# Optimization experiments

Measured on AMD Instinct MI355X. Metric: run time of the kernel, lower is better.

Reference implementation:

```python
import jax, jax.numpy as jnp
import numpy as np

BN_EPS = 1e-5

def setup_inputs() -> dict:
    key = jax.random.key(0)
    ks = jax.random.split(key, 6)
    B, C, H, W, K = 16, 512, 64, 64, 32
    return {
        "x": jax.random.normal(ks[0], (B, C, H, W), dtype=jnp.float32),
        "conv_w": jax.random.normal(ks[1], (C, C), dtype=jnp.float32) * (1.0 / np.sqrt(C)),
        "conv_b": jax.random.normal(ks[2], (C,), dtype=jnp.float32) * 0.01,
        "codewords": jax.random.normal(ks[3], (K, C), dtype=jnp.float32) * (1.0 / np.sqrt(C)),
        "scale": jax.random.uniform(ks[4], (K,), dtype=jnp.float32, minval=-1.0, maxval=0.0),
        "bn_gamma": jnp.ones((K,), jnp.float32),
        "bn_beta": jnp.zeros((K,), jnp.float32),
        "bn_mean": jnp.zeros((K,), jnp.float32),
        "bn_var": jnp.ones((K,), jnp.float32),
        "fc_w": jax.random.normal(ks[5], (C, C), dtype=jnp.float32) * (1.0 / np.sqrt(C)),
        "fc_b": jnp.zeros((C,), jnp.float32),
    }

def reference(x, conv_w, conv_b, codewords, scale, bn_gamma, bn_beta, bn_mean, bn_var, fc_w, fc_b):
    B, C, H, W = x.shape
    N = H * W
    # 1x1 conv projection: (B,C,H,W) x (O,C) -> (B,O,H,W)
    proj = jnp.einsum('bchw,oc->bohw', x, conv_w) + conv_b[None, :, None, None]
    z = proj.reshape(B, C, N).transpose(0, 2, 1)  # (B, N, C)
    # scaled L2 distances without materializing (B,N,K,C):
    # ||z - cw||^2 = ||z||^2 - 2 z.cw + ||cw||^2
    z_sq = jnp.sum(z * z, axis=-1)                     # (B, N)
    cw_sq = jnp.sum(codewords * codewords, axis=-1)    # (K,)
    cross = jnp.einsum('bnc,kc->bnk', z, codewords)    # (B, N, K)
    dist = scale[None, None, :] * (z_sq[:, :, None] - 2.0 * cross + cw_sq[None, None, :])
    assign = jax.nn.softmax(dist, axis=2)              # (B, N, K)
    # aggregate: sum_n a[b,n,k] * (z[b,n,c] - cw[k,c])
    enc = jnp.einsum('bnk,bnc->bkc', assign, z) - jnp.sum(assign, axis=1)[:, :, None] * codewords[None]  # (B, K, C)
    # BatchNorm1d(num_codes) in eval mode normalizes the K (feature) axis, then ReLU
    inv_std = jax.lax.rsqrt(bn_var + BN_EPS)
    enc_bn = (enc - bn_mean[None, :, None]) * (inv_std * bn_gamma)[None, :, None] + bn_beta[None, :, None]
    encoding_feat = jnp.mean(jax.nn.relu(enc_bn), axis=1)  # (B, C)
    # sigmoid channel gate + residual fuse
    gamma = jax.nn.sigmoid(encoding_feat @ fc_w.T + fc_b)  # (B, C)
    y = gamma[:, :, None, None]
    output = jax.nn.relu(x + x * y)
    return (encoding_feat, output)
```

## Files before the change

### kernel.cpp

```cpp
#include <hip/hip_runtime.h>
#include <hip/hip_bf16.h>
#include <stdint.h>

#define DEV static __device__ __forceinline__

typedef __attribute__((ext_vector_type(8))) short bf16x8;
typedef __attribute__((ext_vector_type(4))) float f32x4;

DEV void async_ld16(const void* g, void* l) {
  __builtin_amdgcn_global_load_lds(
      (const __attribute__((address_space(1))) void*)g,
      (__attribute__((address_space(3))) void*)l, 16, 0, 0);
}

DEV unsigned short f2bf(float f) {
  union { __hip_bfloat16 h; unsigned short u; } c;
  c.h = __float2bfloat16(f);
  return c.u;
}

#define Bb 16
#define Cc 512
#define Nn 4096
#define Kk 32
#define NSPLIT 32

__global__ void k_castw(const float* __restrict__ a, __hip_bfloat16* __restrict__ o) {
  int i = blockIdx.x * 256 + threadIdx.x;
  o[i] = __float2bfloat16(a[i]);
}

__global__ void k_cw(const float* __restrict__ cw, __hip_bfloat16* __restrict__ cwb,
                     float* __restrict__ cwsq) {
  int k = blockIdx.x, lane = threadIdx.x;
  float s = 0.f;
#pragma unroll
  for (int j = 0; j < 8; ++j) {
    float v = cw[k * Cc + lane * 8 + j];
    cwb[k * Cc + lane * 8 + j] = __float2bfloat16(v);
    s += v * v;
  }
  for (int off = 32; off; off >>= 1) s += __shfl_down(s, off);
  if (lane == 0) cwsq[k] = s;
}

__global__ __launch_bounds__(256) void k_gemm_z(const float* __restrict__ X,
                                                const __hip_bfloat16* __restrict__ Bw,
                                                const float* __restrict__ bias,
                                                __hip_bfloat16* __restrict__ Z) {
  constexpr int LDA = 36;
  __shared__ __align__(16) unsigned short As[128 * LDA];
  __shared__ __align__(16) __hip_bfloat16 Bs[128 * 32];
  const int b = blockIdx.y;
  const int n0 = (blockIdx.x & 31) * 128;
  const int c0 = (blockIdx.x >> 5) * 128;
  const int tid = threadIdx.x;
  const int lane = tid & 63, wid = tid >> 6;
  const int wr = (wid >> 1) * 64, wc = (wid & 1) * 64;
  const int cg = tid & 7;
  const int ng = tid >> 3;
  const float* Xb = X + (size_t)b * Cc * Nn + n0 + ng * 4;
  const __hip_bfloat16* Bbp = Bw + (size_t)c0 * Cc;
  f32x4 acc[4][4] = {};
  for (int kt = 0; kt < 16; ++kt) {
    int k0 = kt * 32;
    __syncthreads();
#pragma unroll
    for (int j = 0; j < 2; ++j) {
      int li = tid + j * 256;
      int row = li >> 2, kc = (li & 3) * 8;
      async_ld16(Bbp + (size_t)row * Cc + k0 + kc, (char*)Bs + li * 16);
    }
    float vv[4][4];
#pragma unroll
    for (int i = 0; i < 4; ++i) {
      float4 t = *(const float4*)&Xb[(size_t)(k0 + cg * 4 + i) * Nn];
      vv[i][0] = t.x; vv[i][1] = t.y; vv[i][2] = t.z; vv[i][3] = t.w;
    }
#pragma unroll
    for (int j = 0; j < 4; ++j) {
      ushort4 w;
      w.x = f2bf(vv[0][j]);
      w.y = f2bf(vv[1][j]);
      w.z = f2bf(vv[2][j]);
      w.w = f2bf(vv[3][j]);
      *(ushort4*)&As[(ng * 4 + j) * LDA + cg * 4] = w;
    }
    __syncthreads();
    bf16x8 af[4], bfv[4];
#pragma unroll
    for (int m = 0; m < 4; ++m) {
      int base = (wr + m * 16 + (lane & 15)) * LDA + (lane >> 4) * 8;
      union { ushort4 u2[2]; bf16x8 v8; } t;
      t.u2[0] = *(const ushort4*)&As[base];
      t.u2[1] = *(const ushort4*)&As[base + 4];
      af[m] = t.v8;
    }
#pragma unroll
    for (int nf = 0; nf < 4; ++nf)
      bfv[nf] = *(const bf16x8*)&Bs[(wc + nf * 16 + (lane & 15)) * 32 + (lane >> 4) * 8];
#pragma unroll
    for (int m = 0; m < 4; ++m)
#pragma unroll
      for (int nf = 0; nf < 4; ++nf)
        acc[m][nf] = __builtin_amdgcn_mfma_f32_16x16x32_bf16(af[m], bfv[nf], acc[m][nf], 0, 0, 0);
  }
  __hip_bfloat16* Zb = Z + ((size_t)b * Nn + n0) * Cc + c0;
#pragma unroll
  for (int nf = 0; nf < 4; ++nf) {
    int col = wc + nf * 16 + (lane & 15);
    float bv = bias[c0 + col];
#pragma unroll
    for (int m = 0; m < 4; ++m) {
#pragma unroll
      for (int r = 0; r < 4; ++r) {
        int row = wr + m * 16 + (lane >> 4) * 4 + r;
        Zb[(size_t)row * Cc + col] = __float2bfloat16(acc[m][nf][r] + bv);
      }
    }
  }
}

__global__ __launch_bounds__(256) void k_cross(const __hip_bfloat16* __restrict__ Z,
                                               const __hip_bfloat16* __restrict__ CW,
                                               const float* __restrict__ scale,
                                               const float* __restrict__ cwsq,
                                               float* __restrict__ assign,
                                               float* __restrict__ asum) {
  __shared__ __align__(16) __hip_bfloat16 As[128 * 32];
  __shared__ __align__(16) __hip_bfloat16 Bs[32 * 32];
  __shared__ float s_zsq[128];
  __shared__ float s_asum[Kk];
  int b = blockIdx.y;
  int n0 = blockIdx.x * 128;
  int tid = threadIdx.x, lane = tid & 63, wid = tid >> 6;
  if (tid < Kk) s_asum[tid] = 0.f;
  const __hip_bfloat16* Ab = Z + ((size_t)b * Nn + n0) * Cc;
  f32x4 acc[2][2] = {};
  float sq = 0.f;
  for (int kt = 0; kt < 16; ++kt) {
    int k0 = kt * 32;
    __syncthreads();
#pragma unroll
    for (int j = 0; j < 2; ++j) {
      int li = tid + j * 256;
      int row = li >> 2, kc = (li & 3) * 8;
      async_ld16(Ab + (size_t)row * Cc + k0 + kc, (char*)As + li * 16);
    }
    if (tid < 128) {
      int row = tid >> 2, kc = (tid & 3) * 8;
      async_ld16(CW + (size_t)row * Cc + k0 + kc, (char*)Bs + tid * 16);
    }
    __syncthreads();
    {
      int row = tid >> 1, h = (tid & 1) * 16;
      const __hip_bfloat16* p = &As[row * 32 + h];
#pragma unroll
      for (int i = 0; i < 16; ++i) {
        float v = __bfloat162float(p[i]);
        sq += v * v;
      }
    }
    bf16x8 af[2], bfv[2];
#pragma unroll
    for (int m = 0; m < 2; ++m)
      af[m] = *(const bf16x8*)&As[(wid * 32 + m * 16 + (lane & 15)) * 32 + (lane >> 4) * 8];
#pragma unroll
    for (int nf = 0; nf < 2; ++nf)
      bfv[nf] = *(const bf16x8*)&Bs[(nf * 16 + (lane & 15)) * 32 + (lane >> 4) * 8];
#pragma unroll
    for (int m = 0; m < 2; ++m)
#pragma unroll
      for (int nf = 0; nf < 2; ++nf)
        acc[m][nf] = __builtin_amdgcn_mfma_f32_16x16x32_bf16(af[m], bfv[nf], acc[m][nf], 0, 0, 0);
  }
  sq += __shfl_xor(sq, 1);
  if ((tid & 1) == 0) s_zsq[tid >> 1] = sq;
  __syncthreads();
  float sc[2], cq[2];
#pragma unroll
  for (int nf = 0; nf < 2; ++nf) {
    sc[nf] = scale[nf * 16 + (lane & 15)];
    cq[nf] = cwsq[nf * 16 + (lane & 15)];
  }
  float asump0 = 0.f, asump1 = 0.f;
#pragma unroll
  for (int m = 0; m < 2; ++m) {
#pragma unroll
    for (int r = 0; r < 4; ++r) {
      int row = wid * 32 + m * 16 + (lane >> 4) * 4 + r;
      float zq = s_zsq[row];
      float v0 = sc[0] * (zq - 2.f * acc[m][0][r] + cq[0]);
      float v1 = sc[1] * (zq - 2.f * acc[m][1][r] + cq[1]);
      float mx = fmaxf(v0, v1);
#pragma unroll
      for (int off = 1; off < 16; off <<= 1) mx = fmaxf(mx, __shfl_xor(mx, off));
      float e0 = __expf(v0 - mx), e1 = __expf(v1 - mx);
      float s = e0 + e1;
#pragma unroll
      for (int off = 1; off < 16; off <<= 1) s += __shfl_xor(s, off);
      float inv = 1.f / s;
      float a0 = e0 * inv, a1 = e1 * inv;
      acc[m][0][r] = a0;
      acc[m][1][r] = a1;
      asump0 += a0;
      asump1 += a1;
    }
  }
  asump0 += __shfl_xor(asump0, 16); asump0 += __shfl_xor(asump0, 32);
  asump1 += __shfl_xor(asump1, 16); asump1 += __shfl_xor(asump1, 32);
  if (lane < 16) {
    atomicAdd(&s_asum[lane], asump0);
    atomicAdd(&s_asum[16 + lane], asump1);
  }
  float* Cb = assign + ((size_t)b * Nn + n0) * Kk;
#pragma unroll
  for (int m = 0; m < 2; ++m)
#pragma unroll
    for (int nf = 0; nf < 2; ++nf) {
      int col = nf * 16 + (lane & 15);
#pragma unroll
      for (int r = 0; r < 4; ++r) {
        int row = wid * 32 + m * 16 + (lane >> 4) * 4 + r;
        Cb[(size_t)row * Kk + col] = acc[m][nf][r];
      }
    }
  __syncthreads();
  if (tid < Kk) atomicAdd(&asum[b * Kk + tid], s_asum[tid]);
}

__global__ __launch_bounds__(256) void k_enc_part(const float* __restrict__ assign,
                                                  const __hip_bfloat16* __restrict__ Z,
                                                  float* __restrict__ part) {
  __shared__ float sa[128][Kk];
  int b = blockIdx.z;
  int s = blockIdx.y;
  int c = blockIdx.x * 256 + threadIdx.x;
  int tid = threadIdx.x;
  int n0 = s * 128;
  const float* ap = assign + ((size_t)b * Nn + n0) * Kk;
  for (int i = tid; i < 128 * Kk; i += 256) sa[i >> 5][i & 31] = ap[i];
  __syncthreads();
  float acc[Kk];
#pragma unroll
  for (int k = 0; k < Kk; ++k) acc[k] = 0.f;
  const __hip_bfloat16* zp = Z + ((size_t)b * Nn + n0) * Cc + c;
  for (int n = 0; n < 128; ++n) {
    float zv = __bfloat162float(zp[(size_t)n * Cc]);
    const float4* sp = (const float4*)&sa[n][0];
#pragma unroll
    for (int q = 0; q < 8; ++q) {
      float4 a4 = sp[q];
      acc[4 * q + 0] = fmaf(a4.x, zv, acc[4 * q + 0]);
      acc[4 * q + 1] = fmaf(a4.y, zv, acc[4 * q + 1]);
      acc[4 * q + 2] = fmaf(a4.z, zv, acc[4 * q + 2]);
      acc[4 * q + 3] = fmaf(a4.w, zv, acc[4 * q + 3]);
    }
  }
  float* pp = part + (((size_t)s * Bb + b) * Kk) * Cc + c;
#pragma unroll
  for (int k = 0; k < Kk; ++k) pp[(size_t)k * Cc] = acc[k];
}

__global__ __launch_bounds__(256) void k_enc_bn(const float* __restrict__ part,
                                                const float* __restrict__ asum,
                                                const float* __restrict__ cw,
                                                const float* __restrict__ bn_g,
                                                const float* __restrict__ bn_b,
                                                const float* __restrict__ bn_m,
                                                const float* __restrict__ bn_v,
                                                float* __restrict__ ef) {
  int bk = blockIdx.x;
  int b = bk >> 5, k = bk & 31;
  int tid = threadIdx.x;
  float g = bn_g[k], bt = bn_b[k], mn = bn_m[k], iv = rsqrtf(bn_v[k] + 1e-5f);
  float as = asum[bk];
  for (int c = tid; c < Cc; c += 256) {
    float e = 0.f;
#pragma unroll
    for (int s = 0; s < NSPLIT; ++s)
      e += part[(((size_t)s * Bb + b) * Kk + k) * Cc + c];
    e -= as * cw[k * Cc + c];
    e = (e - mn) * (iv * g) + bt;
    e = fmaxf(e, 0.f);
    atomicAdd(&ef[b * Cc + c], e * (1.f / 32.f));
  }
}

__global__ void k_fc(const float* __restrict__ ef, const float* __restrict__ fcw,
                     const float* __restrict__ fcb, float* __restrict__ gamma) {
  int b = blockIdx.x;
  int o = blockIdx.y * 4 + (threadIdx.x >> 6);
  int lane = threadIdx.x & 63;
  const float* w = fcw + (size_t)o * Cc;
  const float* e = ef + b * Cc;
  float s = 0.f;
#pragma unroll
  for (int j = 0; j < 8; ++j) s += e[lane + j * 64] * w[lane + j * 64];
  for (int off = 32; off; off >>= 1) s += __shfl_down(s, off);
  if (lane == 0) gamma[b * Cc + o] = 1.f / (1.f + __expf(-(s + fcb[o])));
}

__global__ __launch_bounds__(256) void k_out(const float* __restrict__ x,
                                             const float* __restrict__ gamma,
                                             float* __restrict__ out) {
  int bc = blockIdx.x;
  float m = 1.f + gamma[bc];
  size_t base = (size_t)bc * (Nn / 4);
  const float4* xp = (const float4*)x + base;
  float4* op = (float4*)out + base;
#pragma unroll
  for (int j = 0; j < 4; ++j) {
    int i = j * 256 + threadIdx.x;
    float4 v = xp[i];
    float4 r;
    r.x = fmaxf(v.x * m, 0.f);
    r.y = fmaxf(v.y * m, 0.f);
    r.z = fmaxf(v.z * m, 0.f);
    r.w = fmaxf(v.w * m, 0.f);
    op[i] = r;
  }
}

extern "C" void kernel_launch(void* const* d_in, const int* in_sizes, int n_in,
                              void* d_out, int out_size, void* d_ws, size_t ws_size,
                              hipStream_t stream) {
  const float* x = (const float*)d_in[0];
  const float* conv_w = (const float*)d_in[1];
  const float* conv_b = (const float*)d_in[2];
  const float* codewords = (const float*)d_in[3];
  const float* scale = (const float*)d_in[4];
  const float* bn_gamma = (const float*)d_in[5];
  const float* bn_beta = (const float*)d_in[6];
  const float* bn_mean = (const float*)d_in[7];
  const float* bn_var = (const float*)d_in[8];
  const float* fc_w = (const float*)d_in[9];
  const float* fc_b = (const float*)d_in[10];

  float* ef_out = (float*)d_out;
  float* out = (float*)d_out + Bb * Cc;

  char* ws = (char*)d_ws;
  size_t off = 0;
  float* part = (float*)(ws + off);
  off += (size_t)NSPLIT * Bb * Kk * Cc * 4;
  __hip_bfloat16* z = (__hip_bfloat16*)(ws + off);
  off += (size_t)Bb * Nn * Cc * 2;
  float* assign = (float*)(ws + off);
  off += (size_t)Bb * Nn * Kk * 4;
  __hip_bfloat16* wbf = (__hip_bfloat16*)(ws + off);
  off += (size_t)Cc * Cc * 2;
  __hip_bfloat16* cwb = (__hip_bfloat16*)(ws + off);
  off += (size_t)Kk * Cc * 2;
  float* cwsq = (float*)(ws + off);
  off += 512;
  float* asum = (float*)(ws + off);
  off += (size_t)Bb * Kk * 4;
  float* gamma = (float*)(ws + off);
  off += (size_t)Bb * Cc * 4;
  (void)ws_size; (void)n_in; (void)in_sizes; (void)out_size;

  hipMemsetAsync(asum, 0, Bb * Kk * 4, stream);
  hipMemsetAsync(ef_out, 0, Bb * Cc * 4, stream);

  k_castw<<<dim3(Cc * Cc / 256), dim3(256), 0, stream>>>(conv_w, wbf);
  k_cw<<<dim3(Kk), dim3(64), 0, stream>>>(codewords, cwb, cwsq);
  k_gemm_z<<<dim3((Nn / 128) * 4, Bb), dim3(256), 0, stream>>>(x, wbf, conv_b, z);
  k_cross<<<dim3(Nn / 128, Bb), dim3(256), 0, stream>>>(z, cwb, scale, cwsq, assign, asum);
  k_enc_part<<<dim3(Cc / 256, NSPLIT, Bb), dim3(256), 0, stream>>>(assign, z, part);
  k_enc_bn<<<dim3(Bb * Kk), dim3(256), 0, stream>>>(part, asum, codewords, bn_gamma, bn_beta,
                                                    bn_mean, bn_var, ef_out);
  k_fc<<<dim3(Bb, Cc / 4), dim3(256), 0, stream>>>(ef_out, fc_w, fc_b, gamma);
  k_out<<<dim3(Bb * Cc), dim3(256), 0, stream>>>(x, gamma, out);
}
```

Measured before the change: 213.0 us.

## Double-buffer LDS tiles and prefetch next X tile in projection GEMM

Adds double-buffered LDS for the A and B tiles of the projection GEMM and prefetches the next K-slice of X into registers while MFMAs run on the current buffer. This drops one barrier per iteration and overlaps global loads with compute. The thread-to-data mapping for X loads also changes (cg/ng swapped), so each row read spans 32 consecutive float4s for better coalescing. In exchange, LDS use doubles, which may lower occupancy, and register pressure rises from the prefetched values.

```diff
diff --git a/kernel.cpp b/kernel.cpp
--- a/kernel.cpp
+++ b/kernel.cpp
@@ -49,61 +49,70 @@
                                                 const float* __restrict__ bias,
                                                 __hip_bfloat16* __restrict__ Z) {
   constexpr int LDA = 36;
-  __shared__ __align__(16) unsigned short As[128 * LDA];
-  __shared__ __align__(16) __hip_bfloat16 Bs[128 * 32];
+  constexpr int AE = 128 * LDA;
+  constexpr int BE = 128 * 32;
+  __shared__ __align__(16) unsigned short As[2 * AE];
+  __shared__ __align__(16) __hip_bfloat16 Bs[2 * BE];
   const int b = blockIdx.y;
   const int n0 = (blockIdx.x & 31) * 128;
   const int c0 = (blockIdx.x >> 5) * 128;
   const int tid = threadIdx.x;
   const int lane = tid & 63, wid = tid >> 6;
   const int wr = (wid >> 1) * 64, wc = (wid & 1) * 64;
-  const int cg = tid & 7;
-  const int ng = tid >> 3;
+  const int cg = tid >> 5;
+  const int ng = tid & 31;
   const float* Xb = X + (size_t)b * Cc * Nn + n0 + ng * 4;
   const __hip_bfloat16* Bbp = Bw + (size_t)c0 * Cc;
   f32x4 acc[4][4] = {};
+  float4 av[4];
+#pragma unroll
+  for (int i = 0; i < 4; ++i)
+    av[i] = *(const float4*)&Xb[(size_t)(cg * 4 + i) * Nn];
+  int cur = 0;
   for (int kt = 0; kt < 16; ++kt) {
-    int k0 = kt * 32;
-    __syncthreads();
+    unsigned short* Aw = As + cur * AE;
+#pragma unroll
+    for (int j = 0; j < 4; ++j) {
+      ushort4 w;
+      w.x = f2bf(av[0][j]);
+      w.y = f2bf(av[1][j]);
+      w.z = f2bf(av[2][j]);
+      w.w = f2bf(av[3][j]);
+      *(ushort4*)&Aw[(ng * 4 + j) * LDA + cg * 4] = w;
+    }
+    char* Bwr = (char*)(Bs + cur * BE);
 #pragma unroll
     for (int j = 0; j < 2; ++j) {
       int li = tid + j * 256;
       int row = li >> 2, kc = (li & 3) * 8;
-      async_ld16(Bbp + (size_t)row * Cc + k0 + kc, (char*)Bs + li * 16);
-    }
-    float vv[4][4];
-#pragma unroll
-    for (int i = 0; i < 4; ++i) {
-      float4 t = *(const float4*)&Xb[(size_t)(k0 + cg * 4 + i) * Nn];
-      vv[i][0] = t.x; vv[i][1] = t.y; vv[i][2] = t.z; vv[i][3] = t.w;
-    }
-#pragma unroll
-    for (int j = 0; j < 4; ++j) {
-      ushort4 w;
-      w.x = f2bf(vv[0][j]);
-      w.y = f2bf(vv[1][j]);
-      w.z = f2bf(vv[2][j]);
-      w.w = f2bf(vv[3][j]);
-      *(ushort4*)&As[(ng * 4 + j) * LDA + cg * 4] = w;
+      async_ld16(Bbp + (size_t)row * Cc + kt * 32 + kc, Bwr + li * 16);
     }
     __syncthreads();
+    if (kt < 15) {
+#pragma unroll
+      for (int i = 0; i < 4; ++i)
+        av[i] = *(const float4*)&Xb[(size_t)((kt + 1) * 32 + cg * 4 + i) * Nn];
+    }
+    const unsigned short* Ar = As + cur * AE;
+    const __hip_bfloat16* Br = Bs + cur * BE;
     bf16x8 af[4], bfv[4];
 #pragma unroll
     for (int m = 0; m < 4; ++m) {
       int base = (wr + m * 16 + (lane & 15)) * LDA + (lane >> 4) * 8;
       union { ushort4 u2[2]; bf16x8 v8; } t;
-      t.u2[0] = *(const ushort4*)&As[base];
-      t.u2[1] = *(const ushort4*)&As[base + 4];
+      t.u2[0] = *(const ushort4*)&Ar[base];
+      t.u2[1] = *(const ushort4*)&Ar[base + 4];
       af[m] = t.v8;
     }
 #pragma unroll
     for (int nf = 0; nf < 4; ++nf)
-      bfv[nf] = *(const bf16x8*)&Bs[(wc + nf * 16 + (lane & 15)) * 32 + (lane >> 4) * 8];
+      bfv[nf] = *(const bf16x8*)&Br[(wc + nf * 16 + (lane & 15)) * 32 + (lane >> 4) * 8];
 #pragma unroll
     for (int m = 0; m < 4; ++m)
 #pragma unroll
       for (int nf = 0; nf < 4; ++nf)
         acc[m][nf] = __builtin_amdgcn_mfma_f32_16x16x32_bf16(af[m], bfv[nf], acc[m][nf], 0, 0, 0);
+    cur ^= 1;
   }
   __hip_bfloat16* Zb = Z + ((size_t)b * Nn + n0) * Cc + c0;
 #pragma unroll
```

After: 185.8 us. -12.8%, faster.
